# Kernel optimization log

Measured on AMD Instinct MI355X. Metric: run time of the kernel, lower is better.

Reference implementation:

```python
import jax, jax.numpy as jnp
import numpy as np

NUM_HEADS = 16


def setup_inputs() -> dict:
    key = jax.random.key(0)
    ks = jax.random.split(key, 4)
    B, T, E = 4, 2048, 1024
    x = jax.random.normal(ks[0], (B, T, E), dtype=jnp.float32)
    # orthogonal-ish init approximated by scaled normal; values don't affect math checks
    W_qkv = jax.random.normal(ks[1], (E, 3 * E), dtype=jnp.float32) * (1.0 / np.sqrt(E))
    b_qkv = jnp.zeros((3 * E,), dtype=jnp.float32)
    W_out = jax.random.normal(ks[2], (E, E), dtype=jnp.float32) * (1.0 / np.sqrt(E))
    b_out = jnp.zeros((E,), dtype=jnp.float32)
    return {"x": x, "W_qkv": W_qkv, "b_qkv": b_qkv, "W_out": W_out, "b_out": b_out}


def reference(x, W_qkv, b_qkv, W_out, b_out):
    B, T, E = x.shape
    H = NUM_HEADS
    hd = E // H
    qkv = x @ W_qkv + b_qkv                     # [B,T,3E]
    q, k, v = jnp.split(qkv, 3, axis=-1)
    # [B,T,E] -> [B,H,T,hd]
    q = q.reshape(B, T, H, hd).transpose(0, 2, 1, 3)
    k = k.reshape(B, T, H, hd).transpose(0, 2, 1, 3)
    v = v.reshape(B, T, H, hd).transpose(0, 2, 1, 3)
    scale = 1.0 / jnp.sqrt(jnp.float32(hd))
    attn = jnp.einsum("bhqd,bhkd->bhqk", q, k) * scale
    causal = jnp.tril(jnp.ones((T, T), dtype=bool))[None, None]
    attn = jnp.where(causal, attn, -jnp.inf)
    attn = jax.nn.softmax(attn, axis=-1)
    y = jnp.einsum("bhqk,bhkd->bhqd", attn, v)   # [B,H,T,hd]
    y = y.transpose(0, 2, 1, 3).reshape(B, T, E)
    return y @ W_out + b_out
```

## Files before the change

kernel.cpp:

```cpp
#include <hip/hip_runtime.h>
#include <cstdint>
#include <cstddef>

using v8s  = __attribute__((ext_vector_type(8))) short;
using v4f  = __attribute__((ext_vector_type(4))) float;

#define MFMA(a, b, c) __builtin_amdgcn_mfma_f32_16x16x32_bf16(a, b, c, 0, 0, 0)
#define AS1(p) (const __attribute__((address_space(1))) void*)(p)
#define AS3(p) (__attribute__((address_space(3))) void*)(p)

__device__ __forceinline__ unsigned short f2bf(float f) {
    unsigned int u = __float_as_uint(f);
    unsigned int r = (u + 0x7fffu + ((u >> 16) & 1u)) >> 16;
    return (unsigned short)r;
}

__global__ __launch_bounds__(256) void cast_x_kernel(const float* __restrict__ x,
                                                     unsigned short* __restrict__ xb) {
    size_t i = ((size_t)blockIdx.x * 256 + threadIdx.x) * 8;
    float4 a = *reinterpret_cast<const float4*>(x + i);
    float4 b = *reinterpret_cast<const float4*>(x + i + 4);
    union { unsigned short u[8]; v8s v; } o;
    o.u[0] = f2bf(a.x); o.u[1] = f2bf(a.y); o.u[2] = f2bf(a.z); o.u[3] = f2bf(a.w);
    o.u[4] = f2bf(b.x); o.u[5] = f2bf(b.y); o.u[6] = f2bf(b.z); o.u[7] = f2bf(b.w);
    *reinterpret_cast<v8s*>(xb + i) = o.v;
}

__global__ __launch_bounds__(256) void transpose_w_kernel(const float* __restrict__ W,
                                                          unsigned short* __restrict__ Wt,
                                                          int Kd, int Nd) {
    __shared__ float tile[32][33];
    int tx = threadIdx.x, ty = threadIdx.y;
    int n0 = blockIdx.x * 32, k0 = blockIdx.y * 32;
#pragma unroll
    for (int i = 0; i < 4; ++i)
        tile[ty + i * 8][tx] = W[(size_t)(k0 + ty + i * 8) * Nd + (n0 + tx)];
    __syncthreads();
#pragma unroll
    for (int i = 0; i < 4; ++i)
        Wt[(size_t)(n0 + ty + i * 8) * Kd + (k0 + tx)] = f2bf(tile[tx][ty + i * 8]);
}

template <int EPI>
__global__ __launch_bounds__(256, 3) void gemm_bt(const unsigned short* __restrict__ A,
                                                  const unsigned short* __restrict__ Bt,
                                                  const float* __restrict__ bias,
                                                  unsigned short* __restrict__ outq,
                                                  unsigned short* __restrict__ outk,
                                                  unsigned short* __restrict__ outv,
                                                  float* __restrict__ outf) {
    __shared__ unsigned short sA[128 * 64];
    __shared__ unsigned short sB[128 * 64];
    const int tid = threadIdx.x;
    const int lane = tid & 63, wid = tid >> 6;
    const int lr = lane & 15, lg = lane >> 4;
    const int m0 = blockIdx.x * 128, n0 = blockIdx.y * 128;
    const int wr = wid >> 1, wc = wid & 1;

    v4f acc[4][4] = {};

    int srow[4], scol[4];
#pragma unroll
    for (int j = 0; j < 4; ++j) {
        int o = j * 4096 + tid * 16;
        int row = o >> 7, cb = o & 127;
        srow[j] = row;
        scol[j] = (cb ^ ((row & 7) << 4)) >> 1;
    }

    for (int kt = 0; kt < 16; ++kt) {
        __syncthreads();
#pragma unroll
        for (int j = 0; j < 4; ++j) {
            const unsigned short* ga = A + (size_t)(m0 + srow[j]) * 1024 + kt * 64 + scol[j];
            __builtin_amdgcn_global_load_lds(AS1(ga), AS3((char*)sA + j * 4096 + wid * 1024), 16, 0, 0);
            const unsigned short* gb = Bt + (size_t)(n0 + srow[j]) * 1024 + kt * 64 + scol[j];
            __builtin_amdgcn_global_load_lds(AS1(gb), AS3((char*)sB + j * 4096 + wid * 1024), 16, 0, 0);
        }
        __syncthreads();

        v8s af[4][2], bf[4][2];
#pragma unroll
        for (int m = 0; m < 4; ++m) {
            int row = wr * 64 + m * 16 + lr;
#pragma unroll
            for (int kk = 0; kk < 2; ++kk) {
                int c = (kk * 64 + lg * 16) ^ ((row & 7) << 4);
                af[m][kk] = *reinterpret_cast<const v8s*>((const char*)sA + row * 128 + c);
            }
        }
#pragma unroll
        for (int n = 0; n < 4; ++n) {
            int row = wc * 64 + n * 16 + lr;
#pragma unroll
            for (int kk = 0; kk < 2; ++kk) {
                int c = (kk * 64 + lg * 16) ^ ((row & 7) << 4);
                bf[n][kk] = *reinterpret_cast<const v8s*>((const char*)sB + row * 128 + c);
            }
        }
#pragma unroll
        for (int m = 0; m < 4; ++m)
#pragma unroll
            for (int n = 0; n < 4; ++n) {
                acc[m][n] = MFMA(af[m][0], bf[n][0], acc[m][n]);
                acc[m][n] = MFMA(af[m][1], bf[n][1], acc[m][n]);
            }
    }

#pragma unroll
    for (int m = 0; m < 4; ++m) {
        int rowb = m0 + wr * 64 + m * 16 + lg * 4;
#pragma unroll
        for (int n = 0; n < 4; ++n) {
            int gn = n0 + wc * 64 + n * 16 + lr;
            float bs = bias[gn];
            if (EPI == 0) {
                int which = gn >> 10, e = gn & 1023;
                int h = e >> 6, d = e & 63;
#pragma unroll
                for (int r = 0; r < 4; ++r) {
                    int grow = rowb + r;
                    int b = grow >> 11, t = grow & 2047;
                    size_t bh = (size_t)(b * 16 + h);
                    float v = acc[m][n][r] + bs;
                    if (which == 0)
                        outq[(bh * 2048 + t) * 64 + d] = f2bf(v * 0.125f);
                    else if (which == 1)
                        outk[(bh * 2048 + t) * 64 + d] = f2bf(v);
                    else
                        outv[(bh * 64 + d) * 2048 + t] = f2bf(v);
                }
            } else {
#pragma unroll
                for (int r = 0; r < 4; ++r)
                    outf[(size_t)(rowb + r) * 1024 + gn] = acc[m][n][r] + bs;
            }
        }
    }
}

__global__ __launch_bounds__(256, 4) void attn_kernel(const unsigned short* __restrict__ qb,
                                                      const unsigned short* __restrict__ kb,
                                                      const unsigned short* __restrict__ vT,
                                                      unsigned short* __restrict__ yb) {
    __shared__ unsigned short sK[2][64 * 64];
    __shared__ unsigned short sV[2][64 * 64];
    __shared__ unsigned short pbuf[4][16 * 64];

    const int tid = threadIdx.x;
    const int lane = tid & 63, wid = tid >> 6;
    const int lr = lane & 15, lg = lane >> 4;

    const int bid = blockIdx.x;
    const int o = (bid & 7) * 256 + (bid >> 3);
    const int bh = o >> 5;
    const int qt = 31 - (o & 31);

    const unsigned short* Q  = qb + (size_t)bh * 2048 * 64;
    const unsigned short* Kp = kb + (size_t)bh * 2048 * 64;
    const unsigned short* Vt = vT + (size_t)bh * 64 * 2048;

    const int q0 = qt * 64 + wid * 16;
    v8s qf0 = *reinterpret_cast<const v8s*>(Q + (size_t)(q0 + lr) * 64 + lg * 8);
    v8s qf1 = *reinterpret_cast<const v8s*>(Q + (size_t)(q0 + lr) * 64 + 32 + lg * 8);

    int strow[2], stcol[2];
#pragma unroll
    for (int it = 0; it < 2; ++it) {
        int os = it * 4096 + tid * 16;
        int row = os >> 7, cb = os & 127;
        strow[it] = row;
        stcol[it] = (cb ^ ((row & 7) << 4)) >> 1;
    }

    auto stage = [&](int buf, int kv0) {
#pragma unroll
        for (int it = 0; it < 2; ++it) {
            int os = it * 4096 + tid * 16;
            __builtin_amdgcn_global_load_lds(
                AS1(Kp + (size_t)(kv0 + strow[it]) * 64 + stcol[it]),
                AS3((char*)sK[buf] + os), 16, 0, 0);
            __builtin_amdgcn_global_load_lds(
                AS1(Vt + (size_t)strow[it] * 2048 + kv0 + stcol[it]),
                AS3((char*)sV[buf] + os), 16, 0, 0);
        }
    };

    float mrow = -1e30f, lrow = 0.f;
    v4f yacc[4] = {};

    stage(0, 0);
    int cur = 0;
    for (int kt = 0; kt <= qt; ++kt) {
        __syncthreads();
        if (kt < qt) stage(cur ^ 1, (kt + 1) * 64);

        v4f sacc[4] = {};
#pragma unroll
        for (int j = 0; j < 4; ++j) {
            int row = j * 16 + lr;
            int sw = (row & 7) << 4;
            v8s kf0 = *reinterpret_cast<const v8s*>((const char*)sK[cur] + row * 128 + ((lg * 16) ^ sw));
            v8s kf1 = *reinterpret_cast<const v8s*>((const char*)sK[cur] + row * 128 + ((64 + lg * 16) ^ sw));
            sacc[j] = MFMA(kf0, qf0, sacc[j]);
            sacc[j] = MFMA(kf1, qf1, sacc[j]);
        }

        if (kt == qt) {
            const int qq = q0 + lr;
            const int kv0 = kt * 64;
#pragma unroll
            for (int j = 0; j < 4; ++j)
#pragma unroll
                for (int r = 0; r < 4; ++r)
                    if (kv0 + j * 16 + lg * 4 + r > qq) sacc[j][r] = -1e30f;
        }

        float tmax = -1e30f;
#pragma unroll
        for (int j = 0; j < 4; ++j)
            tmax = fmaxf(tmax, fmaxf(fmaxf(sacc[j][0], sacc[j][1]), fmaxf(sacc[j][2], sacc[j][3])));
        tmax = fmaxf(tmax, __shfl_xor(tmax, 16, 64));
        tmax = fmaxf(tmax, __shfl_xor(tmax, 32, 64));
        float newm = fmaxf(mrow, tmax);
        float sc = __expf(mrow - newm);
        mrow = newm;
        float ps = 0.f;
#pragma unroll
        for (int j = 0; j < 4; ++j)
#pragma unroll
            for (int r = 0; r < 4; ++r) {
                float p = __expf(sacc[j][r] - newm);
                sacc[j][r] = p;
                ps += p;
            }
        ps += __shfl_xor(ps, 16, 64);
        ps += __shfl_xor(ps, 32, 64);
        lrow = lrow * sc + ps;

        float scq[4];
#pragma unroll
        for (int r = 0; r < 4; ++r) scq[r] = __shfl(sc, lg * 4 + r, 64);
#pragma unroll
        for (int n = 0; n < 4; ++n)
#pragma unroll
            for (int r = 0; r < 4; ++r) yacc[n][r] *= scq[r];

        unsigned short* pw = pbuf[wid];
#pragma unroll
        for (int j = 0; j < 4; ++j)
#pragma unroll
            for (int r = 0; r < 4; r += 2) {
                int c = j * 16 + lg * 4 + r;
                unsigned int pk = (unsigned int)f2bf(sacc[j][r]) |
                                  ((unsigned int)f2bf(sacc[j][r + 1]) << 16);
                *reinterpret_cast<unsigned int*>(&pw[lr * 64 + (c ^ ((lr & 7) << 3))]) = pk;
            }

        const char* pb = (const char*)pbuf[wid];
        v8s pf0 = *reinterpret_cast<const v8s*>(pb + lr * 128 + ((lg * 16) ^ ((lr & 7) << 4)));
        v8s pf1 = *reinterpret_cast<const v8s*>(pb + lr * 128 + ((64 + lg * 16) ^ ((lr & 7) << 4)));
#pragma unroll
        for (int n = 0; n < 4; ++n) {
            int row = n * 16 + lr;
            int sw = (row & 7) << 4;
            v8s vf0 = *reinterpret_cast<const v8s*>((const char*)sV[cur] + row * 128 + ((lg * 16) ^ sw));
            v8s vf1 = *reinterpret_cast<const v8s*>((const char*)sV[cur] + row * 128 + ((64 + lg * 16) ^ sw));
            yacc[n] = MFMA(pf0, vf0, yacc[n]);
            yacc[n] = MFMA(pf1, vf1, yacc[n]);
        }
        cur ^= 1;
    }

    float inv = 1.0f / lrow;
    float invq[4];
#pragma unroll
    for (int r = 0; r < 4; ++r) invq[r] = __shfl(inv, lg * 4 + r, 64);

    const int b = bh >> 4, h = bh & 15;
#pragma unroll
    for (int r = 0; r < 4; ++r) {
        int t = q0 + lg * 4 + r;
#pragma unroll
        for (int n = 0; n < 4; ++n)
            yb[((size_t)b * 2048 + t) * 1024 + h * 64 + n * 16 + lr] = f2bf(yacc[n][r] * invq[r]);
    }
}

extern "C" void kernel_launch(void* const* d_in, const int* in_sizes, int n_in,
                              void* d_out, int out_size, void* d_ws, size_t ws_size,
                              hipStream_t stream) {
    const float* x     = (const float*)d_in[0];
    const float* W_qkv = (const float*)d_in[1];
    const float* b_qkv = (const float*)d_in[2];
    const float* W_out = (const float*)d_in[3];
    const float* b_out = (const float*)d_in[4];
    float* out = (float*)d_out;

    if (ws_size < (72ull << 20)) return;

    char* ws = (char*)d_ws;
    unsigned short* xb_yb = (unsigned short*)(ws);
    unsigned short* qbf   = (unsigned short*)(ws + (16ull << 20));
    unsigned short* kbf   = (unsigned short*)(ws + (32ull << 20));
    unsigned short* vTb   = (unsigned short*)(ws + (48ull << 20));
    unsigned short* wqkvT = (unsigned short*)(ws + (64ull << 20));
    unsigned short* woutT = (unsigned short*)(ws + (70ull << 20));

    cast_x_kernel<<<dim3(4096), dim3(256), 0, stream>>>(x, xb_yb);
    transpose_w_kernel<<<dim3(96, 32), dim3(32, 8), 0, stream>>>(W_qkv, wqkvT, 1024, 3072);
    transpose_w_kernel<<<dim3(32, 32), dim3(32, 8), 0, stream>>>(W_out, woutT, 1024, 1024);
    gemm_bt<0><<<dim3(64, 24), dim3(256), 0, stream>>>(xb_yb, wqkvT, b_qkv, qbf, kbf, vTb, nullptr);
    attn_kernel<<<dim3(2048), dim3(256), 0, stream>>>(qbf, kbf, vTb, xb_yb);
    gemm_bt<1><<<dim3(64, 8), dim3(256), 0, stream>>>(xb_yb, woutT, b_out, nullptr, nullptr, nullptr, out);
}
```

Measured before the change: 274.6 us.

## Use 128-row query tiles with 8 waves sharing K/V tiles in attention

The attention kernel now runs 512-thread blocks that each cover 128 query rows, with 8 waves sharing every staged 64-row K/V tile, so each K/V tile is loaded once for twice as many queries. The grid is halved, the per-thread staging loop is simplified, and the causal mask is applied per wave whenever a tile overlaps that wave's rows. The bf16 packing of probabilities also switches to the hardware v_cvt_pk_bf16_f32 instruction. The cost is extra work: the lower waves in each block still run the full tile loop on fully masked tiles. Larger blocks also change occupancy and the load balance across the causal triangle.

```diff
diff --git a/kernel.cpp b/kernel.cpp
--- a/kernel.cpp
+++ b/kernel.cpp
@@ -139,61 +139,53 @@
     }
 }
 
-__global__ __launch_bounds__(256, 4) void attn_kernel(const unsigned short* __restrict__ qb,
+__global__ __launch_bounds__(512, 6) void attn_kernel(const unsigned short* __restrict__ qb,
                                                       const unsigned short* __restrict__ kb,
                                                       const unsigned short* __restrict__ vT,
                                                       unsigned short* __restrict__ yb) {
     __shared__ unsigned short sK[2][64 * 64];
     __shared__ unsigned short sV[2][64 * 64];
-    __shared__ unsigned short pbuf[4][16 * 64];
+    __shared__ unsigned short pbuf[8][16 * 64];
 
     const int tid = threadIdx.x;
     const int lane = tid & 63, wid = tid >> 6;
     const int lr = lane & 15, lg = lane >> 4;
 
     const int bid = blockIdx.x;
-    const int o = (bid & 7) * 256 + (bid >> 3);
-    const int bh = o >> 5;
-    const int qt = 31 - (o & 31);
+    const int o = (bid & 7) * 128 + (bid >> 3);
+    const int bh = o >> 4;
+    const int qt = 15 - (o & 15);
 
     const unsigned short* Q  = qb + (size_t)bh * 2048 * 64;
     const unsigned short* Kp = kb + (size_t)bh * 2048 * 64;
     const unsigned short* Vt = vT + (size_t)bh * 64 * 2048;
 
-    const int q0 = qt * 64 + wid * 16;
+    const int q0 = qt * 128 + wid * 16;
     v8s qf0 = *reinterpret_cast<const v8s*>(Q + (size_t)(q0 + lr) * 64 + lg * 8);
     v8s qf1 = *reinterpret_cast<const v8s*>(Q + (size_t)(q0 + lr) * 64 + 32 + lg * 8);
 
-    int strow[2], stcol[2];
-#pragma unroll
-    for (int it = 0; it < 2; ++it) {
-        int os = it * 4096 + tid * 16;
-        int row = os >> 7, cb = os & 127;
-        strow[it] = row;
-        stcol[it] = (cb ^ ((row & 7) << 4)) >> 1;
-    }
+    const int sos   = tid * 16;
+    const int strow = sos >> 7;
+    const int stcol = ((sos & 127) ^ ((strow & 7) << 4)) >> 1;
 
     auto stage = [&](int buf, int kv0) {
-#pragma unroll
-        for (int it = 0; it < 2; ++it) {
-            int os = it * 4096 + tid * 16;
-            __builtin_amdgcn_global_load_lds(
-                AS1(Kp + (size_t)(kv0 + strow[it]) * 64 + stcol[it]),
-                AS3((char*)sK[buf] + os), 16, 0, 0);
-            __builtin_amdgcn_global_load_lds(
-                AS1(Vt + (size_t)strow[it] * 2048 + kv0 + stcol[it]),
-                AS3((char*)sV[buf] + os), 16, 0, 0);
-        }
+        __builtin_amdgcn_global_load_lds(
+            AS1(Kp + (size_t)(kv0 + strow) * 64 + stcol),
+            AS3((char*)sK[buf] + sos), 16, 0, 0);
+        __builtin_amdgcn_global_load_lds(
+            AS1(Vt + (size_t)strow * 2048 + kv0 + stcol),
+            AS3((char*)sV[buf] + sos), 16, 0, 0);
     };
 
     float mrow = -1e30f, lrow = 0.f;
     v4f yacc[4] = {};
 
+    const int ntiles = 2 * qt + 2;
     stage(0, 0);
     int cur = 0;
-    for (int kt = 0; kt <= qt; ++kt) {
+    for (int kt = 0; kt < ntiles; ++kt) {
         __syncthreads();
-        if (kt < qt) stage(cur ^ 1, (kt + 1) * 64);
+        if (kt + 1 < ntiles) stage(cur ^ 1, (kt + 1) * 64);
 
         v4f sacc[4] = {};
 #pragma unroll
@@ -206,9 +198,9 @@
             sacc[j] = MFMA(kf1, qf1, sacc[j]);
         }
 
-        if (kt == qt) {
+        const int kv0 = kt * 64;
+        if (kv0 + 63 > q0) {
             const int qq = q0 + lr;
-            const int kv0 = kt * 64;
 #pragma unroll
             for (int j = 0; j < 4; ++j)
 #pragma unroll
@@ -252,8 +244,9 @@
 #pragma unroll
             for (int r = 0; r < 4; r += 2) {
                 int c = j * 16 + lg * 4 + r;
-                unsigned int pk = (unsigned int)f2bf(sacc[j][r]) |
-                                  ((unsigned int)f2bf(sacc[j][r + 1]) << 16);
+                unsigned int pk;
+                asm("v_cvt_pk_bf16_f32 %0, %1, %2"
+                    : "=v"(pk) : "v"(sacc[j][r]), "v"(sacc[j][r + 1]));
                 *reinterpret_cast<unsigned int*>(&pw[lr * 64 + (c ^ ((lr & 7) << 3))]) = pk;
             }
 
@@ -311,6 +304,6 @@
     transpose_w_kernel<<<dim3(96, 32), dim3(32, 8), 0, stream>>>(W_qkv, wqkvT, 1024, 3072);
     transpose_w_kernel<<<dim3(32, 32), dim3(32, 8), 0, stream>>>(W_out, woutT, 1024, 1024);
     gemm_bt<0><<<dim3(64, 24), dim3(256), 0, stream>>>(xb_yb, wqkvT, b_qkv, qbf, kbf, vTb, nullptr);
-    attn_kernel<<<dim3(2048), dim3(256), 0, stream>>>(qbf, kbf, vTb, xb_yb);
+    attn_kernel<<<dim3(1024), dim3(512), 0, stream>>>(qbf, kbf, vTb, xb_yb);
     gemm_bt<1><<<dim3(64, 8), dim3(256), 0, stream>>>(xb_yb, woutT, b_out, nullptr, nullptr, nullptr, out);
 }
```

Result: no change. 270.7 us (-1.4%).
